# Optimization experiments

Measured on AMD Instinct MI355X. Metric: run time of the kernel, lower is better.

## Reference

```python
import jax, jax.numpy as jnp
import numpy as np

B, T, D, C = 16, 2048, 512, 20
K_EASY, K_HARD = 40, 20
M_BIG, M_SMALL = 7, 3
A4 = A5 = A6 = A7 = 1.0
EPS = 1e-05
DROP_P = 0.6


def setup_inputs() -> dict:
    key = jax.random.key(0)
    ks = jax.random.split(key, 6)
    attn = jax.random.uniform(ks[0], (B, T, 1), dtype=jnp.float32)
    mu = jax.random.normal(ks[1], (B, T, D), dtype=jnp.float32)
    var = jax.random.uniform(ks[2], (B, T, D), dtype=jnp.float32) * 0.9 + 0.1
    mu_clip = jax.random.normal(ks[3], (B, T, D), dtype=jnp.float32)
    text_feat = jax.random.normal(ks[4], (C, D), dtype=jnp.float32)
    keep = (jax.random.uniform(ks[5], (B, T)) >= DROP_P).astype(jnp.float32)
    drop_mask = keep / (1.0 - DROP_P)  # inverted-dropout mask on a ones tensor
    return dict(attn=attn, mu=mu, var=var, mu_clip=mu_clip, text_feat=text_feat, drop_mask=drop_mask)


def _normalize(x, axis=-1):
    n = jnp.linalg.norm(x, axis=axis, keepdims=True)
    return x / jnp.maximum(n, 1e-12)


def _select_topk(scores, emb, k):
    # torch: sort desc, take first k indices, gather along time dim
    _, idx = jax.lax.top_k(scores, k)  # [B,k]
    return jnp.take_along_axis(emb, idx[:, :, None], axis=1)  # [B,k,D]


def _window_reduce(x, w, op_min):
    # binary erosion/dilation along time with structure ones((1,w)), border_value=0
    lo, hi = w // 2, w - 1 - w // 2
    xp = jnp.pad(x, ((0, 0), (lo, hi)), constant_values=0.0)
    if op_min:
        return jax.lax.reduce_window(xp, jnp.inf, jax.lax.min, (1, w), (1, 1), 'VALID')
    return jax.lax.reduce_window(xp, -jnp.inf, jax.lax.max, (1, w), (1, 1), 'VALID')


def _kl_distance(mu_p, cov_p, mu_q, cov_q):
    # vectorized over all (i in k_p) x (j in k_q) pairs
    cov_p = cov_p + EPS
    cov_q = cov_q + EPS
    d = mu_p.shape[-1]
    diff = mu_q[:, None, :, :] - mu_p[:, :, None, :]        # [B,kp,kq,D]
    term1 = 0.5 * jnp.sum(diff * diff / cov_q[:, None, :, :], axis=-1)
    term2 = 0.5 * (jnp.sum(jnp.log(cov_q), -1)[:, None, :] - jnp.sum(jnp.log(cov_p), -1)[:, :, None])
    term3 = 0.5 * jnp.sum(cov_p[:, :, None, :] / cov_q[:, None, :, :], axis=-1)
    dist = term1 + term2 + term3 - 0.5 * d
    return jnp.mean(1.0 / (dist + 1.0), axis=(1, 2))        # [B]


def _prob_contrastive(hard_q, easy_pos, easy_neg):
    pos = _kl_distance(hard_q[0], hard_q[1], easy_pos[0], easy_pos[1])
    neg = _kl_distance(hard_q[0], hard_q[1], easy_neg[0], easy_neg[1])
    return jnp.mean(-(jnp.log(pos) + jnp.log(1.0 - neg)))


def _forward(attn, mu, var, mu_clip, text_feat, drop_mask):
    a = attn[..., 0]                                        # [B,T]
    a_drop = a * drop_mask
    a_rev = jnp.max(a, axis=1, keepdims=True) - a
    a_rev_drop = a_rev * drop_mask
    easy_act = (_select_topk(a_drop, mu, K_EASY), _select_topk(a_drop, var, K_EASY))
    easy_bkg = (_select_topk(a_rev_drop, mu, K_EASY), _select_topk(a_rev_drop, var, K_EASY))

    med = jnp.median(a, axis=1, keepdims=True)
    abin = jnp.where(a > med, 1.0, 0.0)
    er_M = _window_reduce(abin, M_BIG, True)
    er_m = _window_reduce(abin, M_SMALL, True)
    inner = jax.lax.stop_gradient(er_m - er_M)              # mask computed on detached numpy in torch
    dl_m = _window_reduce(abin, M_SMALL, False)
    dl_M = _window_reduce(abin, M_BIG, False)
    outer = jax.lax.stop_gradient(dl_M - dl_m)
    a_inner = a * inner
    a_outer = a * outer
    hard_act = (_select_topk(a_inner, mu, K_HARD), _select_topk(a_inner, var, K_HARD))
    hard_bkg = (_select_topk(a_outer, mu, K_HARD), _select_topk(a_outer, var, K_HARD))

    # Distillation
    sim = jnp.einsum('btd,btd->bt', _normalize(mu), _normalize(mu_clip))
    distill = A4 * (-jnp.log(jnp.mean((sim + 1.0) / 2.0)))

    act_loss = A5 * _prob_contrastive(hard_act, easy_act, easy_bkg)
    bkg_loss = A6 * _prob_contrastive(hard_bkg, easy_bkg, easy_act)

    emb = _normalize(text_feat)
    sim_m = emb @ jax.lax.stop_gradient(emb.T) - jnp.eye(emb.shape[0], dtype=emb.dtype)
    ortho = A7 * jnp.linalg.norm(sim_m)

    total = distill + act_loss + bkg_loss + ortho
    return total, distill, act_loss, bkg_loss, ortho


def reference(attn, mu, var, mu_clip, text_feat, drop_mask):
    return _forward(attn, mu, var, mu_clip, text_feat, drop_mask)
```

## Files before the change

### kernel.cpp

```cpp
#include <hip/hip_runtime.h>
#include <math.h>


#define BB 16
#define TT 2048
#define DD 512
#define CC 20
#define KEASY 40
#define KHARD 20
#define EPSF 1e-5f

typedef unsigned long long u64;

template <int CTRL>
__device__ __forceinline__ float dpp_mov(float x) {
  return __int_as_float(__builtin_amdgcn_update_dpp(
      0, __float_as_int(x), CTRL, 0xF, 0xF, true));
}
template <int CTRL, int RM>
__device__ __forceinline__ unsigned dpp_movu(unsigned x) {
  return (unsigned)__builtin_amdgcn_update_dpp(0, (int)x, CTRL, RM, 0xF, true);
}
__device__ __forceinline__ float wsum63(float v) {
  v += dpp_mov<0x111>(v);
  v += dpp_mov<0x112>(v);
  v += dpp_mov<0x114>(v);
  v += dpp_mov<0x118>(v);
  v += dpp_mov<0x142>(v);
  v += dpp_mov<0x143>(v);
  return v;
}
__device__ __forceinline__ float wsum_bc(float v) {
  return __int_as_float(__builtin_amdgcn_readlane(__float_as_int(wsum63(v)), 63));
}
__device__ __forceinline__ float wmax63(float v) {
  v = fmaxf(v, dpp_mov<0x111>(v));
  v = fmaxf(v, dpp_mov<0x112>(v));
  v = fmaxf(v, dpp_mov<0x114>(v));
  v = fmaxf(v, dpp_mov<0x118>(v));
  v = fmaxf(v, dpp_mov<0x142>(v));
  v = fmaxf(v, dpp_mov<0x143>(v));
  return v;
}
__device__ __forceinline__ unsigned wscanu(unsigned v) {
  v += dpp_movu<0x111, 0xF>(v);
  v += dpp_movu<0x112, 0xF>(v);
  v += dpp_movu<0x114, 0xF>(v);
  v += dpp_movu<0x118, 0xF>(v);
  v += dpp_movu<0x142, 0xa>(v);
  v += dpp_movu<0x143, 0xc>(v);
  return v;
}

__device__ __forceinline__ float radix_kth(const float* sbuf, unsigned k,
                                           unsigned* s_hist4, unsigned* s_state,
                                           int tid, int wid) {
#pragma unroll 1
  for (int round = 0; round < 4; ++round) {
    s_hist4[tid] = 0;
    s_hist4[256 + tid] = 0;
    s_hist4[512 + tid] = 0;
    s_hist4[768 + tid] = 0;
    if (round == 0 && tid == 0) { s_state[0] = 0u; s_state[1] = k; }
    __syncthreads();
    const int shift = 24 - 8 * round;
    const unsigned mask_hi = (round == 0) ? 0u : (0xFFFFFFFFu << (shift + 8));
    const unsigned pref = s_state[0];
    const unsigned kk = s_state[1];
    unsigned* myhist = s_hist4 + (wid << 8);
    unsigned curbin = 0xFFFFFFFFu, curc = 0;
    for (int i = tid; i < TT; i += 256) {
      const unsigned key = __float_as_uint(sbuf[i]);
      if ((key & mask_hi) == pref) {
        const unsigned bin = 255u - ((key >> shift) & 255u);
        if (bin == curbin) {
          curc++;
        } else {
          if (curc) atomicAdd(&myhist[curbin], curc);
          curbin = bin;
          curc = 1;
        }
      }
    }
    if (curc) atomicAdd(&myhist[curbin], curc);
    __syncthreads();
    if (tid < 64) {
      const uint4 h0 = *(const uint4*)(s_hist4 + 4 * tid);
      const uint4 h1 = *(const uint4*)(s_hist4 + 256 + 4 * tid);
      const uint4 h2 = *(const uint4*)(s_hist4 + 512 + 4 * tid);
      const uint4 h3 = *(const uint4*)(s_hist4 + 768 + 4 * tid);
      const unsigned b0 = h0.x + h1.x + h2.x + h3.x;
      const unsigned b1 = h0.y + h1.y + h2.y + h3.y;
      const unsigned b2 = h0.z + h1.z + h2.z + h3.z;
      const unsigned b3 = h0.w + h1.w + h2.w + h3.w;
      const unsigned s0 = b0, s1 = s0 + b1, s2 = s1 + b2, s3 = s2 + b3;
      const unsigned P = wscanu(s3);
      const unsigned E = P - s3;
      const u64 bal = __ballot(P >= kk);
      const int L = (int)__ffsll(bal) - 1;
      if (tid == L) {
        unsigned binj, cb;
        if (E + s0 >= kk)      { binj = 0u; cb = E; }
        else if (E + s1 >= kk) { binj = 1u; cb = E + s0; }
        else if (E + s2 >= kk) { binj = 2u; cb = E + s1; }
        else                   { binj = 3u; cb = E + s2; }
        const unsigned digit = 255u - (4u * (unsigned)tid + binj);
        s_state[0] = pref | (digit << shift);
        s_state[1] = kk - cb;
      }
    }
    __syncthreads();
  }
  return __uint_as_float(s_state[0]);
}

__global__ __launch_bounds__(256, 2) void k_sel(const float* __restrict__ attn,
                                                const float* __restrict__ drop,
                                                const float* __restrict__ var,
                                                int* __restrict__ idxb,
                                                float* __restrict__ slogb) {
  const int tid = threadIdx.x, wid = tid >> 6, lane = tid & 63;
  __shared__ float s_a[TT];
  __shared__ float s_v[TT];
  __shared__ __align__(16) unsigned s_hist4[1024];
  __shared__ unsigned s_state[2];
  __shared__ float s_bc[4];
  __shared__ unsigned s_bcu[4];
  __shared__ int s_idx[KEASY];

  const int b = blockIdx.x >> 2, sel = blockIdx.x & 3;
  for (int i = tid; i < TT; i += 256) s_a[i] = attn[b * TT + i];
  __syncthreads();

  float med = 0.f, mx = 0.f;
  if (sel == 1) {
    float lm = 0.f;
    for (int i = tid; i < TT; i += 256) lm = fmaxf(lm, s_a[i]);
    lm = wmax63(lm);
    if (lane == 63) s_bc[wid] = lm;
    __syncthreads();
    mx = fmaxf(fmaxf(s_bc[0], s_bc[1]), fmaxf(s_bc[2], s_bc[3]));
  } else if (sel >= 2) {
    const float v1 = radix_kth(s_a, 1024u, s_hist4, s_state, tid, wid);
    unsigned c = 0;
    float m2 = 0.f;
    for (int i = tid; i < TT; i += 256) {
      const float x = s_a[i];
      c += (x >= v1) ? 1u : 0u;
      m2 = (x < v1) ? fmaxf(m2, x) : m2;
    }
    c = wscanu(c);
    m2 = wmax63(m2);
    if (lane == 63) { s_bc[wid] = m2; s_bcu[wid] = c; }
    __syncthreads();
    const unsigned ctot = s_bcu[0] + s_bcu[1] + s_bcu[2] + s_bcu[3];
    const float m2t = fmaxf(fmaxf(s_bc[0], s_bc[1]), fmaxf(s_bc[2], s_bc[3]));
    const float v2 = (ctot >= 1025u) ? v1 : m2t;
    med = 0.5f * (v1 + v2);
  }

  for (int i = tid; i < TT; i += 256) {
    const float a = s_a[i];
    float score;
    if (sel == 0) {
      score = a * drop[b * TT + i];
    } else if (sel == 1) {
      score = (mx - a) * drop[b * TT + i];
    } else {
      bool sall = true, ball = true, sany = false, bany = false;
#pragma unroll
      for (int o = -3; o <= 3; o++) {
        const int t = i + o;
        const bool one = (t >= 0 && t < TT) ? (s_a[t] > med) : false;
        if (o >= -1 && o <= 1) { sall = sall && one; sany = sany || one; }
        ball = ball && one;
        bany = bany || one;
      }
      score = (sel == 2) ? ((sall && !ball) ? a : 0.f)
                         : ((bany && !sany) ? a : 0.f);
    }
    s_v[i] = score;
  }
  const unsigned K = (sel < 2) ? KEASY : KHARD;
  const float thr = radix_kth(s_v, K, s_hist4, s_state, tid, wid);

  if (tid < 64) {
    float v[32];
#pragma unroll
    for (int r = 0; r < 32; r++) v[r] = s_v[r * 64 + lane];
    unsigned cgt = 0;
#pragma unroll
    for (int r = 0; r < 32; r++) cgt += (unsigned)__popcll(__ballot(v[r] > thr));
    unsigned need = (cgt < K) ? (K - cgt) : 0u;
    unsigned base = 0;
    const u64 lmask = (1ull << lane) - 1;
    int* dst = idxb + sel * (BB * KEASY) + b * KEASY;
#pragma unroll
    for (int r = 0; r < 32; r++) {
      const bool gt = v[r] > thr;
      const bool eq = v[r] == thr;
      const u64 beq = __ballot(eq);
      const unsigned neq = (unsigned)__popcll(beq);
      const unsigned take = (need < neq) ? need : neq;
      const bool tk = eq && ((unsigned)__popcll(beq & lmask) < take);
      const u64 bsel = __ballot(gt || tk);
      if (gt || tk) {
        const unsigned pos = base + (unsigned)__popcll(bsel & lmask);
        if (pos < K) {
          dst[pos] = r * 64 + lane;
          s_idx[pos] = r * 64 + lane;
        }
      }
      base += (unsigned)__popcll(bsel);
      need -= take;
    }
  }
  __syncthreads();

  const int Ksel = (sel < 2) ? KEASY : KHARD;
  for (int j = wid; j < Ksel; j += 4) {
    const int t = s_idx[j];
    const float* row = var + ((size_t)b * TT + t) * DD;
    float a2 = 0.f;
#pragma unroll
    for (int c = 0; c < 2; c++) {
      float4 vv = *(const float4*)(row + c * 256 + lane * 4);
      a2 += __logf(vv.x + EPSF) + __logf(vv.y + EPSF) +
            __logf(vv.z + EPSF) + __logf(vv.w + EPSF);
    }
    a2 = wsum63(a2);
    if (lane == 63) slogb[sel * 640 + b * 40 + j] = a2;
  }
}

__global__ __launch_bounds__(256, 2) void k_main2(const float* __restrict__ mu,
                                                  const float* __restrict__ var,
                                                  const float* __restrict__ muc,
                                                  const int* __restrict__ idxb,
                                                  const float* __restrict__ slogb,
                                                  const float* __restrict__ text,
                                                  double* __restrict__ acc,
                                                  float* __restrict__ part) {
  __shared__ __align__(16) float smem[2 * KHARD * DD];
  const int tid = threadIdx.x, wid = tid >> 6, lane = tid & 63;
  const int blk = blockIdx.x;

  if (blk >= 257) {
    float* s_red = smem;
    const int dblk = blk - 257;
    const float* pmu = mu + (size_t)(dblk * 4 + wid) * DD + lane * 4;
    const float* pmc = muc + (size_t)(dblk * 4 + wid) * DD + lane * 4;
    float4 x[8], y[8];
#pragma unroll
    for (int j = 0; j < 4; j++) {
      const size_t off = (size_t)j * 8192 * DD;
      x[2 * j]     = *(const float4*)(pmu + off);
      x[2 * j + 1] = *(const float4*)(pmu + off + 256);
      y[2 * j]     = *(const float4*)(pmc + off);
      y[2 * j + 1] = *(const float4*)(pmc + off + 256);
    }
    float wacc = 0.f;
#pragma unroll
    for (int j = 0; j < 4; j++) {
      const float4 cxa = x[2 * j], cxb = x[2 * j + 1];
      const float4 cya = y[2 * j], cyb = y[2 * j + 1];
      float dot = 0.f, n1 = 0.f, n2 = 0.f;
      dot = fmaf(cxa.x, cya.x, fmaf(cxa.y, cya.y, fmaf(cxa.z, cya.z, fmaf(cxa.w, cya.w, dot))));
      n1 = fmaf(cxa.x, cxa.x, fmaf(cxa.y, cxa.y, fmaf(cxa.z, cxa.z, fmaf(cxa.w, cxa.w, n1))));
      n2 = fmaf(cya.x, cya.x, fmaf(cya.y, cya.y, fmaf(cya.z, cya.z, fmaf(cya.w, cya.w, n2))));
      dot = fmaf(cxb.x, cyb.x, fmaf(cxb.y, cyb.y, fmaf(cxb.z, cyb.z, fmaf(cxb.w, cyb.w, dot))));
      n1 = fmaf(cxb.x, cxb.x, fmaf(cxb.y, cxb.y, fmaf(cxb.z, cxb.z, fmaf(cxb.w, cxb.w, n1))));
      n2 = fmaf(cyb.x, cyb.x, fmaf(cyb.y, cyb.y, fmaf(cyb.z, cyb.z, fmaf(cyb.w, cyb.w, n2))));
      dot = wsum63(dot);
      n1 = wsum63(n1);
      n2 = wsum63(n2);
      if (lane == 63) {
        const float sim = dot / (fmaxf(sqrtf(n1), 1e-12f) * fmaxf(sqrtf(n2), 1e-12f));
        wacc += (sim + 1.0f) * 0.5f;
      }
    }
    if (lane == 63) s_red[wid] = wacc;
    __syncthreads();
    if (tid == 0) part[dblk] = s_red[0] + s_red[1] + s_red[2] + s_red[3];
    return;
  }

  if (blk < 256) {
    const int b = blk >> 4, klid = (blk >> 2) & 3, qc = blk & 3;
    const int psel = (klid < 2) ? 2 : 3;
    const int qsel = (klid == 0 || klid == 3) ? 0 : 1;
    float* sP1 = smem;
    float* sP2 = smem + KHARD * DD;
    __shared__ float sSlogP[KHARD];
    __shared__ float s_out[4];
    if (tid < KHARD) sSlogP[tid] = slogb[psel * 640 + b * 40 + tid];
    for (int i = tid; i < KHARD * 128; i += 256) {
      const int p = i >> 7, c = (i & 127) * 4;
      const int t = idxb[psel * 640 + b * 40 + p];
      const size_t base = ((size_t)b * TT + t) * DD + c;
      const float4 m = *(const float4*)(mu + base);
      const float4 vv = *(const float4*)(var + base);
      float4 p1;
      p1.x = fmaf(m.x, m.x, vv.x + EPSF);
      p1.y = fmaf(m.y, m.y, vv.y + EPSF);
      p1.z = fmaf(m.z, m.z, vv.z + EPSF);
      p1.w = fmaf(m.w, m.w, vv.w + EPSF);
      *(float4*)(sP1 + p * DD + c) = p1;
      *(float4*)(sP2 + p * DD + c) = m;
    }
    __syncthreads();

    const int d0 = lane * 4, d1 = 256 + lane * 4;
    const int qbase_i = qsel * 640 + b * 40 + qc * 10;
    float wacc = 0.f;
#pragma unroll 1
    for (int j = wid; j < 10; j += 4) {
      const int qidx = idxb[qbase_i + j];
      const float cslq = slogb[qbase_i + j];
      const float* qm = mu + ((size_t)b * TT + qidx) * DD;
      const float* qv = var + ((size_t)b * TT + qidx) * DD;
      const float4 cma = *(const float4*)(qm + d0);
      const float4 cmb = *(const float4*)(qm + d1);
      const float4 cva = *(const float4*)(qv + d0);
      const float4 cvb = *(const float4*)(qv + d1);
      float4 ra, rb, qra, qrb;
      ra.x = 1.0f / (cva.x + EPSF); ra.y = 1.0f / (cva.y + EPSF);
      ra.z = 1.0f / (cva.z + EPSF); ra.w = 1.0f / (cva.w + EPSF);
      rb.x = 1.0f / (cvb.x + EPSF); rb.y = 1.0f / (cvb.y + EPSF);
      rb.z = 1.0f / (cvb.z + EPSF); rb.w = 1.0f / (cvb.w + EPSF);
      qra.x = cma.x * ra.x; qra.y = cma.y * ra.y;
      qra.z = cma.z * ra.z; qra.w = cma.w * ra.w;
      qrb.x = cmb.x * rb.x; qrb.y = cmb.y * rb.y;
      qrb.z = cmb.z * rb.z; qrb.w = cmb.w * rb.w;
      float cqp = cma.x * qra.x + cma.y * qra.y + cma.z * qra.z + cma.w * qra.w +
                  cmb.x * qrb.x + cmb.y * qrb.y + cmb.z * qrb.z + cmb.w * qrb.w;
      const float cq = wsum63(cqp);
      for (int p = 0; p < KHARD; p++) {
        const float4 p1a = *(const float4*)(sP1 + p * DD + d0);
        const float4 p1b = *(const float4*)(sP1 + p * DD + d1);
        const float4 p2a = *(const float4*)(sP2 + p * DD + d0);
        const float4 p2b = *(const float4*)(sP2 + p * DD + d1);
        const float s1 = p1a.x * ra.x + p1a.y * ra.y + p1a.z * ra.z + p1a.w * ra.w +
                         p1b.x * rb.x + p1b.y * rb.y + p1b.z * rb.z + p1b.w * rb.w;
        const float s2 = p2a.x * qra.x + p2a.y * qra.y + p2a.z * qra.z + p2a.w * qra.w +
                         p2b.x * qrb.x + p2b.y * qrb.y + p2b.z * qrb.z + p2b.w * qrb.w;
        const float h = wsum63(fmaf(0.5f, s1, -s2));
        if (lane == 63) {
          const float dist = h + 0.5f * cq + 0.5f * cslq - 0.5f * sSlogP[p] - 256.0f;
          wacc += 1.0f / (dist + 1.0f);
        }
      }
    }
    if (lane == 63) s_out[wid] = wacc;
    __syncthreads();
    if (tid == 0)
      acc[blk] = (double)s_out[0] + s_out[1] + s_out[2] + s_out[3];
    return;
  }

  {
    float* s_e = smem;
    __shared__ float s_red4[4];
    for (int r = wid; r < CC; r += 4) {
      float4 v[2];
      float ss = 0.f;
#pragma unroll
      for (int c = 0; c < 2; c++) {
        v[c] = *(const float4*)(text + r * DD + c * 256 + lane * 4);
        ss += v[c].x * v[c].x + v[c].y * v[c].y + v[c].z * v[c].z + v[c].w * v[c].w;
      }
      ss = wsum_bc(ss);
      const float n = fmaxf(sqrtf(ss), 1e-12f);
#pragma unroll
      for (int c = 0; c < 2; c++) {
        float4 w = v[c];
        w.x /= n; w.y /= n; w.z /= n; w.w /= n;
        *(float4*)(s_e + r * DD + c * 256 + lane * 4) = w;
      }
    }
    __syncthreads();
    float wss = 0.f;
    for (int p = wid; p < CC * CC; p += 4) {
      const int i = p / CC, j = p % CC;
      float dot = 0.f;
#pragma unroll
      for (int c = 0; c < 2; c++) {
        const int d0 = c * 256 + lane * 4;
        const float4 x = *(const float4*)(s_e + i * DD + d0);
        const float4 y = *(const float4*)(s_e + j * DD + d0);
        dot += x.x * y.x + x.y * y.y + x.z * y.z + x.w * y.w;
      }
      dot = wsum63(dot);
      if (lane == 63) {
        const float s = dot - (i == j ? 1.0f : 0.0f);
        wss += s * s;
      }
    }
    if (lane == 63) s_red4[wid] = wss;
    __syncthreads();
    if (tid == 0)
      acc[256] = (double)(s_red4[0] + s_red4[1] + s_red4[2] + s_red4[3]);
  }
}

__global__ __launch_bounds__(256) void k_final(const double* __restrict__ acc,
                                               const float* __restrict__ part,
                                               float* __restrict__ out) {
  __shared__ double sd[256];
  __shared__ double sla[16], slb[16];
  const int tid = threadIdx.x;
  double s = 0.0;
  for (int i = tid; i < 2048; i += 256) s += (double)part[i];
  sd[tid] = s;
  __syncthreads();
  for (int st = 128; st; st >>= 1) {
    if (tid < st) sd[tid] += sd[tid + st];
    __syncthreads();
  }
  if (tid < 16) {
    const double* ab = acc + tid * 16;
    const double pa = (ab[0] + ab[1] + ab[2] + ab[3]) / 800.0;
    const double na = (ab[4] + ab[5] + ab[6] + ab[7]) / 800.0;
    const double pb = (ab[8] + ab[9] + ab[10] + ab[11]) / 800.0;
    const double nb = (ab[12] + ab[13] + ab[14] + ab[15]) / 800.0;
    sla[tid] = -(log(pa) + log(1.0 - na));
    slb[tid] = -(log(pb) + log(1.0 - nb));
  }
  __syncthreads();
  if (tid == 0) {
    double act = 0.0, bkg = 0.0;
    for (int b = 0; b < 16; b++) { act += sla[b]; bkg += slb[b]; }
    act /= 16.0;
    bkg /= 16.0;
    const double distill = -log(sd[0] / (double)(BB * TT));
    const double ortho = sqrt(acc[256]);
    const double total = distill + act + bkg + ortho;
    out[0] = (float)total;
    out[1] = (float)distill;
    out[2] = (float)act;
    out[3] = (float)bkg;
    out[4] = (float)ortho;
  }
}

extern "C" void kernel_launch(void* const* d_in, const int* in_sizes, int n_in,
                              void* d_out, int out_size, void* d_ws, size_t ws_size,
                              hipStream_t stream) {
  const float* attn = (const float*)d_in[0];
  const float* mu   = (const float*)d_in[1];
  const float* var  = (const float*)d_in[2];
  const float* muc  = (const float*)d_in[3];
  const float* text = (const float*)d_in[4];
  const float* drop = (const float*)d_in[5];
  float* out = (float*)d_out;

  double* acc  = (double*)d_ws;
  int* idxb    = (int*)(acc + 257);
  float* slogb = (float*)(idxb + 2560);
  float* part  = (float*)(slogb + 2560);

  k_sel<<<64, 256, 0, stream>>>(attn, drop, var, idxb, slogb);
  k_main2<<<2305, 256, 0, stream>>>(mu, var, muc, idxb, slogb, text, acc, part);
  k_final<<<1, 256, 0, stream>>>(acc, part, out);
}
```

Baseline: 235.9 us.

## Move distillation streaming into selection kernel to overlap with top-k selection

```diff
diff --git a/kernel.cpp b/kernel.cpp
--- a/kernel.cpp
+++ b/kernel.cpp
@@ -114,12 +114,57 @@
   return __uint_as_float(s_state[0]);
 }
 
-__global__ __launch_bounds__(256, 2) void k_sel(const float* __restrict__ attn,
-                                                const float* __restrict__ drop,
-                                                const float* __restrict__ var,
-                                                int* __restrict__ idxb,
-                                                float* __restrict__ slogb) {
+__global__ __launch_bounds__(256, 2) void k_main1(const float* __restrict__ attn,
+                                                  const float* __restrict__ drop,
+                                                  const float* __restrict__ mu,
+                                                  const float* __restrict__ muc,
+                                                  const float* __restrict__ var,
+                                                  int* __restrict__ idxb,
+                                                  float* __restrict__ slogb,
+                                                  float* __restrict__ part) {
   const int tid = threadIdx.x, wid = tid >> 6, lane = tid & 63;
+
+  if (blockIdx.x >= 64) {
+    __shared__ float s_red[4];
+    const int d = blockIdx.x - 64;
+    const int row0 = d * 16 + wid * 4;
+    const float* pmu = mu + (size_t)row0 * DD + lane * 4;
+    const float* pmc = muc + (size_t)row0 * DD + lane * 4;
+    float4 x[8], y[8];
+#pragma unroll
+    for (int r = 0; r < 4; r++) {
+      const int off = r * DD;
+      x[2 * r]     = *(const float4*)(pmu + off);
+      x[2 * r + 1] = *(const float4*)(pmu + off + 256);
+      y[2 * r]     = *(const float4*)(pmc + off);
+      y[2 * r + 1] = *(const float4*)(pmc + off + 256);
+    }
+    float wacc = 0.f;
+#pragma unroll
+    for (int r = 0; r < 4; r++) {
+      const float4 cxa = x[2 * r], cxb = x[2 * r + 1];
+      const float4 cya = y[2 * r], cyb = y[2 * r + 1];
+      float dot = 0.f, n1 = 0.f, n2 = 0.f;
+      dot = fmaf(cxa.x, cya.x, fmaf(cxa.y, cya.y, fmaf(cxa.z, cya.z, fmaf(cxa.w, cya.w, dot))));
+      n1 = fmaf(cxa.x, cxa.x, fmaf(cxa.y, cxa.y, fmaf(cxa.z, cxa.z, fmaf(cxa.w, cxa.w, n1))));
+      n2 = fmaf(cya.x, cya.x, fmaf(cya.y, cya.y, fmaf(cya.z, cya.z, fmaf(cya.w, cya.w, n2))));
+      dot = fmaf(cxb.x, cyb.x, fmaf(cxb.y, cyb.y, fmaf(cxb.z, cyb.z, fmaf(cxb.w, cyb.w, dot))));
+      n1 = fmaf(cxb.x, cxb.x, fmaf(cxb.y, cxb.y, fmaf(cxb.z, cxb.z, fmaf(cxb.w, cxb.w, n1))));
+      n2 = fmaf(cyb.x, cyb.x, fmaf(cyb.y, cyb.y, fmaf(cyb.z, cyb.z, fmaf(cyb.w, cyb.w, n2))));
+      dot = wsum63(dot);
+      n1 = wsum63(n1);
+      n2 = wsum63(n2);
+      if (lane == 63) {
+        const float sim = dot / (fmaxf(sqrtf(n1), 1e-12f) * fmaxf(sqrtf(n2), 1e-12f));
+        wacc += (sim + 1.0f) * 0.5f;
+      }
+    }
+    if (lane == 63) s_red[wid] = wacc;
+    __syncthreads();
+    if (tid == 0) part[d] = s_red[0] + s_red[1] + s_red[2] + s_red[3];
+    return;
+  }
+
   __shared__ float s_a[TT];
   __shared__ float s_v[TT];
   __shared__ __align__(16) unsigned s_hist4[1024];
@@ -233,57 +278,15 @@
   }
 }
 
-__global__ __launch_bounds__(256, 2) void k_main2(const float* __restrict__ mu,
+__global__ __launch_bounds__(256, 1) void k_part2(const float* __restrict__ mu,
                                                   const float* __restrict__ var,
-                                                  const float* __restrict__ muc,
                                                   const int* __restrict__ idxb,
                                                   const float* __restrict__ slogb,
                                                   const float* __restrict__ text,
-                                                  double* __restrict__ acc,
-                                                  float* __restrict__ part) {
+                                                  double* __restrict__ acc) {
   __shared__ __align__(16) float smem[2 * KHARD * DD];
   const int tid = threadIdx.x, wid = tid >> 6, lane = tid & 63;
   const int blk = blockIdx.x;
-
-  if (blk >= 257) {
-    float* s_red = smem;
-    const int dblk = blk - 257;
-    const float* pmu = mu + (size_t)(dblk * 4 + wid) * DD + lane * 4;
-    const float* pmc = muc + (size_t)(dblk * 4 + wid) * DD + lane * 4;
-    float4 x[8], y[8];
-#pragma unroll
-    for (int j = 0; j < 4; j++) {
-      const size_t off = (size_t)j * 8192 * DD;
-      x[2 * j]     = *(const float4*)(pmu + off);
-      x[2 * j + 1] = *(const float4*)(pmu + off + 256);
-      y[2 * j]     = *(const float4*)(pmc + off);
-      y[2 * j + 1] = *(const float4*)(pmc + off + 256);
-    }
-    float wacc = 0.f;
-#pragma unroll
-    for (int j = 0; j < 4; j++) {
-      const float4 cxa = x[2 * j], cxb = x[2 * j + 1];
-      const float4 cya = y[2 * j], cyb = y[2 * j + 1];
-      float dot = 0.f, n1 = 0.f, n2 = 0.f;
-      dot = fmaf(cxa.x, cya.x, fmaf(cxa.y, cya.y, fmaf(cxa.z, cya.z, fmaf(cxa.w, cya.w, dot))));
-      n1 = fmaf(cxa.x, cxa.x, fmaf(cxa.y, cxa.y, fmaf(cxa.z, cxa.z, fmaf(cxa.w, cxa.w, n1))));
-      n2 = fmaf(cya.x, cya.x, fmaf(cya.y, cya.y, fmaf(cya.z, cya.z, fmaf(cya.w, cya.w, n2))));
-      dot = fmaf(cxb.x, cyb.x, fmaf(cxb.y, cyb.y, fmaf(cxb.z, cyb.z, fmaf(cxb.w, cyb.w, dot))));
-      n1 = fmaf(cxb.x, cxb.x, fmaf(cxb.y, cxb.y, fmaf(cxb.z, cxb.z, fmaf(cxb.w, cxb.w, n1))));
-      n2 = fmaf(cyb.x, cyb.x, fmaf(cyb.y, cyb.y, fmaf(cyb.z, cyb.z, fmaf(cyb.w, cyb.w, n2))));
-      dot = wsum63(dot);
-      n1 = wsum63(n1);
-      n2 = wsum63(n2);
-      if (lane == 63) {
-        const float sim = dot / (fmaxf(sqrtf(n1), 1e-12f) * fmaxf(sqrtf(n2), 1e-12f));
-        wacc += (sim + 1.0f) * 0.5f;
-      }
-    }
-    if (lane == 63) s_red[wid] = wacc;
-    __syncthreads();
-    if (tid == 0) part[dblk] = s_red[0] + s_red[1] + s_red[2] + s_red[3];
-    return;
-  }
 
   if (blk < 256) {
     const int b = blk >> 4, klid = (blk >> 2) & 3, qc = blk & 3;
@@ -459,7 +462,7 @@
   float* slogb = (float*)(idxb + 2560);
   float* part  = (float*)(slogb + 2560);
 
-  k_sel<<<64, 256, 0, stream>>>(attn, drop, var, idxb, slogb);
-  k_main2<<<2305, 256, 0, stream>>>(mu, var, muc, idxb, slogb, text, acc, part);
+  k_main1<<<2112, 256, 0, stream>>>(attn, drop, mu, muc, var, idxb, slogb, part);
+  k_part2<<<257, 256, 0, stream>>>(mu, var, idxb, slogb, text, acc);
   k_final<<<1, 256, 0, stream>>>(acc, part, out);
 }
```

Result: slower. 245.3 us (+4.0%).
